# Kernel optimization log

Hardware: AMD Instinct MI355X
Metric: run time of the kernel (lower is better)

The kernel has to match this reference:

```python
import jax, jax.numpy as jnp
import numpy as np

B, T, D, H = 2, 2048, 2048, 32
HD = D // H
# quantization scales (constructor-time attributes in the original repo)
A_PROJ = 3e-4   # q/k/v proj alpha (W8A8B8O8Linear)
A_QK = 2e-5     # qk_bmm alpha (BMM_S8T_S8N_F32T)
A_PV = 1e-2     # pv_bmm alpha (BMM_S8T_S8N_S8T)
A_OUT = 1e-4    # out_proj alpha (W8A8BFP32OFP32Linear)


def _i8(key, shape):
    return jax.random.randint(key, shape, -128, 128, dtype=jnp.int32).astype(jnp.int8)


def setup_inputs() -> dict:
    key = jax.random.key(0)
    ks = jax.random.split(key, 10)
    hidden_states = _i8(ks[0], (B, T, D))
    # causal mask, 0 on/below diagonal, large negative above
    causal = jnp.triu(jnp.full((T, T), -1e9, dtype=jnp.float32), k=1)
    attention_mask = jnp.broadcast_to(causal, (B, 1, T, T))
    return {
        "hidden_states": hidden_states,
        "attention_mask": attention_mask,
        "Wq": _i8(ks[1], (D, D)), "bq": _i8(ks[2], (D,)),
        "Wk": _i8(ks[3], (D, D)), "bk": _i8(ks[4], (D,)),
        "Wv": _i8(ks[5], (D, D)), "bv": _i8(ks[6], (D,)),
        "Wo": _i8(ks[7], (D, D)),
        "bo": jax.random.normal(ks[8], (D,), dtype=jnp.float32),
    }


def _w8a8b8o8(x_i8, W_i8, b_i8, alpha):
    # int8 GEMM -> int32 accum; epilogue: alpha*acc + bias, saturate to int8
    acc = jnp.einsum('btk,nk->btn', x_i8.astype(jnp.int32), W_i8.astype(jnp.int32))
    y = alpha * acc.astype(jnp.float32) + b_i8.astype(jnp.float32)
    return jnp.clip(jnp.round(y), -128, 127).astype(jnp.int8)


def reference(hidden_states, attention_mask, Wq, bq, Wk, bk, Wv, bv, Wo, bo):
    # q/k/v projections: int8 in, int8 out
    q = _w8a8b8o8(hidden_states, Wq, bq, A_PROJ)
    k = _w8a8b8o8(hidden_states, Wk, bk, A_PROJ)
    v = _w8a8b8o8(hidden_states, Wv, bv, A_PROJ)

    def shape(x):  # [B,T,D] -> [B,H,T,HD]
        return x.reshape(B, T, H, HD).transpose(0, 2, 1, 3)

    qh, kh, vh = shape(q), shape(k), shape(v)

    # qk_bmm (BMM_S8T_S8N_F32T): fp32 = alpha * int8 q @ k^T
    attn = A_QK * jnp.einsum('bhtd,bhsd->bhts',
                             qh.astype(jnp.int32), kh.astype(jnp.int32)).astype(jnp.float32)
    attn = attn + attention_mask  # [B,1,T,T] broadcasts over heads
    attn = jnp.maximum(attn, jnp.finfo(jnp.float32).min)
    probs = jax.nn.softmax(attn, axis=-1)

    # quantize probs: p.mul_(127).round_() -> int8
    p_i8 = jnp.clip(jnp.round(probs * 127.0), -128, 127).astype(jnp.int8)

    # pv_bmm (BMM_S8T_S8N_S8T): int8 out = sat(round(alpha * p @ v))
    pv = jnp.einsum('bhts,bhsd->bhtd', p_i8.astype(jnp.int32), vh.astype(jnp.int32))
    attn_out_i8 = jnp.clip(jnp.round(A_PV * pv.astype(jnp.float32)), -128, 127).astype(jnp.int8)

    # [B,H,T,HD] -> [B,T,D]
    attn_out = attn_out_i8.transpose(0, 2, 1, 3).reshape(B, T, D)

    # out_proj (W8A8BFP32OFP32Linear): fp32 = alpha*(x@W^T) + fp32 bias
    acc = jnp.einsum('btk,nk->btn', attn_out.astype(jnp.int32), Wo.astype(jnp.int32))
    out = A_OUT * acc.astype(jnp.float32) + bo
    return out
```

## Files before the change

kernel.cpp:

```cpp
#include <hip/hip_runtime.h>
#include <cstdint>

#define A_PROJ 3e-4f
#define A_QK   2e-5f
#define A_PV   1e-2f
#define A_OUT  1e-4f

#define NB 2
#define NT 2048
#define ND 2048
#define NH 32
#define NHD 64
#define NM (NB*NT)

typedef int v4i __attribute__((ext_vector_type(4)));

__device__ __forceinline__ int8_t sat8(float y) {
  float r = rintf(y);
  r = fminf(fmaxf(r, -128.f), 127.f);
  return (int8_t)(int)r;
}

__device__ __forceinline__ float exp2_fast(float x) {
  return __builtin_amdgcn_exp2f(x);
}

__device__ __forceinline__ void gl2lds16(const int8_t* g, int8_t* l) {
  __builtin_amdgcn_global_load_lds(
      (const __attribute__((address_space(1))) void*)g,
      (__attribute__((address_space(3))) void*)l, 16, 0, 0);
}

__device__ __forceinline__ uint32_t pack_lo4(float f0, float f1, float f2, float f3) {
  uint32_t u0 = __float_as_uint(f0), u1 = __float_as_uint(f1);
  uint32_t u2 = __float_as_uint(f2), u3 = __float_as_uint(f3);
  uint32_t lo = __builtin_amdgcn_perm(u1, u0, 0x04000400u);
  uint32_t hi = __builtin_amdgcn_perm(u3, u2, 0x04000400u);
  return __builtin_amdgcn_perm(hi, lo, 0x05040100u);
}

#define NWW (ND*ND/4)
__global__ void pack_all(const int* __restrict__ X,
                         const int* __restrict__ W0, const int* __restrict__ W1,
                         const int* __restrict__ W2, const int* __restrict__ W3,
                         int8_t* __restrict__ dX, int8_t* __restrict__ dW0,
                         int8_t* __restrict__ dW1, int8_t* __restrict__ dW2,
                         int8_t* __restrict__ dW3) {
  int i = blockIdx.x * blockDim.x + threadIdx.x;
  const int nx = NM*ND/4;
  const int* src; int8_t* dst; int off;
  if (i < nx) { src = X; dst = dX; off = i; }
  else {
    int j = i - nx;
    int r = j >> 20;
    off = j & (NWW - 1);
    src = (r == 0) ? W0 : (r == 1) ? W1 : (r == 2) ? W2 : W3;
    dst = (r == 0) ? dW0 : (r == 1) ? dW1 : (r == 2) ? dW2 : dW3;
  }
  int4 v = ((const int4*)src)[off];
  uint32_t p = (uint32_t)(v.x & 255) | ((uint32_t)(v.y & 255) << 8) |
               ((uint32_t)(v.z & 255) << 16) | ((uint32_t)(v.w & 255) << 24);
  ((uint32_t*)dst)[off] = p;
}

__global__ __launch_bounds__(256) void gemm_qkv(
    const int8_t* __restrict__ X,
    const int8_t* __restrict__ Wq, const int8_t* __restrict__ Wk, const int8_t* __restrict__ Wv,
    const int* __restrict__ bq, const int* __restrict__ bk, const int* __restrict__ bv,
    int8_t* __restrict__ Qh, int8_t* __restrict__ Kh, int8_t* __restrict__ Vt)
{
  __shared__ __align__(16) int8_t As[2][128][64];
  __shared__ __align__(16) int8_t Bs[2][128][64];
  const int z = blockIdx.z;
  const int8_t* W  = (z == 0) ? Wq : ((z == 1) ? Wk : Wv);
  const int* bias  = (z == 0) ? bq : ((z == 1) ? bk : bv);
  const int m0 = blockIdx.x * 128, n0 = blockIdx.y * 128;
  const int tid = threadIdx.x, lane = tid & 63, wave = tid >> 6;
  const int wm = wave >> 1, wn = wave & 1;
  const int l15 = lane & 15, quad = lane >> 4;

  const int srow = lane >> 2;
  const int scol = (((lane & 3) ^ ((lane >> 3) & 3)) * 16);
  const int rqcol = (quad ^ ((l15 >> 1) & 3)) * 16;

  v4i acc[4][4];
  const v4i vzero = {0, 0, 0, 0};
  #pragma unroll
  for (int i = 0; i < 4; ++i)
    #pragma unroll
    for (int j = 0; j < 4; ++j) acc[i][j] = vzero;

  for (int k0 = 0; k0 < ND; k0 += 128) {
    #pragma unroll
    for (int j = 0; j < 8; ++j) {
      int slot = j * 4 + wave;
      int sl = slot & 15;
      int hh = sl >> 3, rblk = sl & 7;
      int row = rblk * 16 + srow;
      if (slot < 16) {
        gl2lds16(&X[(size_t)(m0 + row) * ND + k0 + hh * 64 + scol], &As[hh][rblk * 16][0]);
      } else {
        gl2lds16(&W[(size_t)(n0 + row) * ND + k0 + hh * 64 + scol], &Bs[hh][rblk * 16][0]);
      }
    }
    __syncthreads();
    #pragma unroll
    for (int hh = 0; hh < 2; ++hh) {
      v4i a[4], b[4];
      #pragma unroll
      for (int mt = 0; mt < 4; ++mt) a[mt] = *(const v4i*)&As[hh][wm*64 + mt*16 + l15][rqcol];
      #pragma unroll
      for (int nt = 0; nt < 4; ++nt) b[nt] = *(const v4i*)&Bs[hh][wn*64 + nt*16 + l15][rqcol];
      #pragma unroll
      for (int mt = 0; mt < 4; ++mt)
        #pragma unroll
        for (int nt = 0; nt < 4; ++nt)
          acc[mt][nt] = __builtin_amdgcn_mfma_i32_16x16x64_i8(a[mt], b[nt], acc[mt][nt], 0, 0, 0);
    }
    __syncthreads();
  }

  float bf[4];
  #pragma unroll
  for (int nt = 0; nt < 4; ++nt) bf[nt] = (float)bias[n0 + wn*64 + nt*16 + l15];

  if (z == 2) {
    #pragma unroll
    for (int mt = 0; mt < 4; ++mt)
      #pragma unroll
      for (int nt = 0; nt < 4; ++nt) {
        int tbase = (m0 + wm*64 + mt*16 + quad*4) & (NT - 1);
        int bb = (m0 + wm*64) >> 11;
        int n = n0 + wn*64 + nt*16 + l15;
        int hh = n >> 6, hd = n & (NHD - 1);
        uint32_t pk = 0;
        #pragma unroll
        for (int r = 0; r < 4; ++r) {
          uint32_t q = (uint32_t)(uint8_t)sat8(A_PROJ * (float)acc[mt][nt][r] + bf[nt]);
          pk |= q << (8 * r);
        }
        size_t bh = (size_t)bb * NH + hh;
        *(uint32_t*)&Vt[(bh * NHD + hd) * NT + tbase] = pk;
      }
  } else {
    int8_t* O = (z == 0) ? Qh : Kh;
    #pragma unroll
    for (int mt = 0; mt < 4; ++mt)
      #pragma unroll
      for (int nt = 0; nt < 4; ++nt)
        #pragma unroll
        for (int r = 0; r < 4; ++r) {
          int m = m0 + wm*64 + mt*16 + quad*4 + r;
          int n = n0 + wn*64 + nt*16 + l15;
          int8_t q = sat8(A_PROJ * (float)acc[mt][nt][r] + bf[nt]);
          int bb = m >> 11, t = m & (NT - 1);
          int hh = n >> 6, hd = n & (NHD - 1);
          size_t bh = (size_t)bb * NH + hh;
          O[(bh * NT + t) * NHD + hd] = q;
        }
  }
}

__global__ __launch_bounds__(512, 8) void attn_fused(
    const int8_t* __restrict__ Qh, const int8_t* __restrict__ Kh, const int8_t* __restrict__ Vt,
    int8_t* __restrict__ AO)
{
  __shared__ __align__(16) uint32_t Ps32[8][16][20];
  __shared__ float Lsh[2][4][16];
  __shared__ __align__(16) v4i Comb[1024];

  const int bx = blockIdx.x;
  const int bh = blockIdx.y;
  const int tid = threadIdx.x, lane = tid & 63, wave = tid >> 6;
  const int wlocal = wave & 3, group = wave >> 2;
  const int l15 = lane & 15, quad = lane >> 4;
  const v4i vzero = {0, 0, 0, 0};
  const float MAGIC = 12582912.0f;
  const float C2 = 2.8853900817779268e-05f;

  const int8_t* Qp = Qh + (size_t)bh * NT * NHD;
  const int8_t* Kp = Kh + (size_t)bh * NT * NHD;
  const int8_t* Vp = Vt + (size_t)bh * NHD * NT;
  const int bb = bh >> 5, hhead = bh & (NH - 1);
  const int soff = group * 64;

  for (int half = 0; half < 2; ++half) {
    const int xq = half ? (31 - bx) : bx;
    const int t0 = xq * 64;
    const int sd = xq >> 1;
    const int tme = t0 + wlocal * 16 + l15;
    const bool gmask = (group == (xq & 1));
    const bool gskip = (group == 1) && !(xq & 1);

    v4i qf = *(const v4i*)&Qp[(size_t)(t0 + wlocal * 16 + l15) * NHD + quad * 16];

    float lsum = 0.f;
    for (int st = 0; st <= sd; ++st) {
      if (st == sd && gskip) continue;
      const int s0 = st * 128;
      const int8_t* kb = &Kp[(size_t)(s0 + soff + l15) * NHD + quad * 16];
      if (st == sd && gmask) {
        #pragma unroll
        for (int mt = 0; mt < 4; ++mt) {
          v4i kf = *(const v4i*)(kb + mt * 16 * NHD);
          v4i sa = __builtin_amdgcn_mfma_i32_16x16x64_i8(kf, qf, vzero, 0, 0, 0);
          const int sbase = s0 + soff + mt*16 + quad*4;
          #pragma unroll
          for (int r = 0; r < 4; ++r) {
            float e = exp2_fast(C2 * (float)sa[r]);
            lsum += (sbase + r <= tme) ? e : 0.f;
          }
        }
      } else {
        #pragma unroll
        for (int mt = 0; mt < 4; ++mt) {
          v4i kf = *(const v4i*)(kb + mt * 16 * NHD);
          v4i sa = __builtin_amdgcn_mfma_i32_16x16x64_i8(kf, qf, vzero, 0, 0, 0);
          #pragma unroll
          for (int r = 0; r < 4; ++r) lsum += exp2_fast(C2 * (float)sa[r]);
        }
      }
    }
    lsum += __shfl_xor(lsum, 16, 64);
    lsum += __shfl_xor(lsum, 32, 64);
    if (quad == 0) Lsh[group][wlocal][l15] = lsum;
    __syncthreads();
    lsum += Lsh[group ^ 1][wlocal][l15];
    const float linv = 127.0f / lsum;

    v4i accv[4];
    #pragma unroll
    for (int j = 0; j < 4; ++j) accv[j] = vzero;

    for (int st = 0; st <= sd; ++st) {
      if (st == sd && gskip) continue;
      const int s0 = st * 128;
      const int8_t* kb = &Kp[(size_t)(s0 + soff + l15) * NHD + quad * 16];

      if (st == sd && gmask) {
        #pragma unroll
        for (int mt = 0; mt < 4; ++mt) {
          v4i kf = *(const v4i*)(kb + mt * 16 * NHD);
          v4i sa = __builtin_amdgcn_mfma_i32_16x16x64_i8(kf, qf, vzero, 0, 0, 0);
          const int sbase = s0 + soff + mt*16 + quad*4;
          float f[4];
          #pragma unroll
          for (int r = 0; r < 4; ++r) {
            float e = (sbase + r <= tme) ? exp2_fast(C2 * (float)sa[r]) : 0.f;
            f[r] = fmaf(e, linv, MAGIC);
          }
          Ps32[wave][l15][mt*4 + quad] = pack_lo4(f[0], f[1], f[2], f[3]);
        }
      } else {
        #pragma unroll
        for (int mt = 0; mt < 4; ++mt) {
          v4i kf = *(const v4i*)(kb + mt * 16 * NHD);
          v4i sa = __builtin_amdgcn_mfma_i32_16x16x64_i8(kf, qf, vzero, 0, 0, 0);
          float f[4];
          #pragma unroll
          for (int r = 0; r < 4; ++r) {
            float e = exp2_fast(C2 * (float)sa[r]);
            f[r] = fmaf(e, linv, MAGIC);
          }
          Ps32[wave][l15][mt*4 + quad] = pack_lo4(f[0], f[1], f[2], f[3]);
        }
      }
      v4i ap = *(const v4i*)&Ps32[wave][l15][quad*4];
      const int8_t* vb = &Vp[(size_t)l15 * NT + s0 + (group*4 + quad) * 16];
      #pragma unroll
      for (int nt2 = 0; nt2 < 4; ++nt2) {
        v4i bvv = *(const v4i*)(vb + (size_t)(nt2 * 16) * NT);
        accv[nt2] = __builtin_amdgcn_mfma_i32_16x16x64_i8(ap, bvv, accv[nt2], 0, 0, 0);
      }
    }

    v4i* AccA = &Comb[0];
    v4i* AccB = &Comb[512];
    const int cbase = (wlocal * 64 + lane) * 2;
    if (group == 1) {
      AccA[cbase + 0] = accv[0];  AccA[cbase + 1] = accv[1];
      AccB[cbase + 0] = accv[2];  AccB[cbase + 1] = accv[3];
    }
    __syncthreads();
    if (group == 0) {
      v4i p0 = AccA[cbase + 0], p1 = AccA[cbase + 1];
      v4i p2 = AccB[cbase + 0], p3 = AccB[cbase + 1];
      accv[0] += p0;  accv[1] += p1;  accv[2] += p2;  accv[3] += p3;
      #pragma unroll
      for (int nt2 = 0; nt2 < 4; ++nt2)
        #pragma unroll
        for (int r = 0; r < 4; ++r) {
          int t = t0 + wlocal*16 + quad*4 + r;
          int d = nt2*16 + l15;
          AO[((size_t)bb * NT + t) * ND + hhead * NHD + d] = sat8(A_PV * (float)accv[nt2][r]);
        }
    }
    __syncthreads();
  }
}

__global__ __launch_bounds__(256) void gemm_out(
    const int8_t* __restrict__ X, const int8_t* __restrict__ W,
    const float* __restrict__ bo, float* __restrict__ out)
{
  __shared__ __align__(16) int8_t As[2][128][64];
  __shared__ __align__(16) int8_t Bs[2][128][64];
  const int m0 = blockIdx.x * 128, n0 = blockIdx.y * 128;
  const int tid = threadIdx.x, lane = tid & 63, wave = tid >> 6;
  const int wm = wave >> 1, wn = wave & 1;
  const int l15 = lane & 15, quad = lane >> 4;
  const int srow = lane >> 2;
  const int scol = (((lane & 3) ^ ((lane >> 3) & 3)) * 16);
  const int rqcol = (quad ^ ((l15 >> 1) & 3)) * 16;

  v4i acc[4][4];
  const v4i vzero = {0, 0, 0, 0};
  #pragma unroll
  for (int i = 0; i < 4; ++i)
    #pragma unroll
    for (int j = 0; j < 4; ++j) acc[i][j] = vzero;

  for (int k0 = 0; k0 < ND; k0 += 128) {
    #pragma unroll
    for (int j = 0; j < 8; ++j) {
      int slot = j * 4 + wave;
      int sl = slot & 15;
      int hh = sl >> 3, rblk = sl & 7;
      int row = rblk * 16 + srow;
      if (slot < 16) {
        gl2lds16(&X[(size_t)(m0 + row) * ND + k0 + hh * 64 + scol], &As[hh][rblk * 16][0]);
      } else {
        gl2lds16(&W[(size_t)(n0 + row) * ND + k0 + hh * 64 + scol], &Bs[hh][rblk * 16][0]);
      }
    }
    __syncthreads();
    #pragma unroll
    for (int hh = 0; hh < 2; ++hh) {
      v4i a[4], b[4];
      #pragma unroll
      for (int mt = 0; mt < 4; ++mt) a[mt] = *(const v4i*)&As[hh][wm*64 + mt*16 + l15][rqcol];
      #pragma unroll
      for (int nt = 0; nt < 4; ++nt) b[nt] = *(const v4i*)&Bs[hh][wn*64 + nt*16 + l15][rqcol];
      #pragma unroll
      for (int mt = 0; mt < 4; ++mt)
        #pragma unroll
        for (int nt = 0; nt < 4; ++nt)
          acc[mt][nt] = __builtin_amdgcn_mfma_i32_16x16x64_i8(a[mt], b[nt], acc[mt][nt], 0, 0, 0);
    }
    __syncthreads();
  }

  float bf[4];
  #pragma unroll
  for (int nt = 0; nt < 4; ++nt) bf[nt] = bo[n0 + wn*64 + nt*16 + l15];

  #pragma unroll
  for (int mt = 0; mt < 4; ++mt)
    #pragma unroll
    for (int nt = 0; nt < 4; ++nt)
      #pragma unroll
      for (int r = 0; r < 4; ++r) {
        int m = m0 + wm*64 + mt*16 + quad*4 + r;
        int n = n0 + wn*64 + nt*16 + l15;
        out[(size_t)m * ND + n] = A_OUT * (float)acc[mt][nt][r] + bf[nt];
      }
}

extern "C" void kernel_launch(void* const* d_in, const int* in_sizes, int n_in,
                              void* d_out, int out_size, void* d_ws, size_t ws_size,
                              hipStream_t stream)
{
  const int*   hs  = (const int*)d_in[0];
  const int*   Wq  = (const int*)d_in[2];
  const int*   bq  = (const int*)d_in[3];
  const int*   Wk  = (const int*)d_in[4];
  const int*   bkb = (const int*)d_in[5];
  const int*   Wv  = (const int*)d_in[6];
  const int*   bvb = (const int*)d_in[7];
  const int*   Wo  = (const int*)d_in[8];
  const float* bo  = (const float*)d_in[9];
  float* out = (float*)d_out;

  char* ws = (char*)d_ws;
  const size_t SZ_X = (size_t)NM * ND;
  const size_t SZ_W = (size_t)ND * ND;
  const size_t SZ_H = (size_t)NB * NH * NT * NHD;
  int8_t* Xp  = (int8_t*)ws;
  int8_t* Wqp = (int8_t*)(ws + SZ_X);
  int8_t* Wkp = Wqp + SZ_W;
  int8_t* Wvp = Wkp + SZ_W;
  int8_t* Wop = Wvp + SZ_W;
  int8_t* Qh  = Wop + SZ_W;
  int8_t* Kh  = Qh + SZ_H;
  int8_t* Vt  = Kh + SZ_H;
  int8_t* AO  = Xp;

  const int ntot = (int)(SZ_X/4 + 4 * (SZ_W/4));
  pack_all<<<(ntot + 255) / 256, 256, 0, stream>>>(hs, Wq, Wk, Wv, Wo,
                                                   Xp, Wqp, Wkp, Wvp, Wop);

  gemm_qkv<<<dim3(NM/128, ND/128, 3), 256, 0, stream>>>(Xp, Wqp, Wkp, Wvp, bq, bkb, bvb, Qh, Kh, Vt);
  attn_fused<<<dim3(16, NB*NH), 512, 0, stream>>>(Qh, Kh, Vt, AO);
  gemm_out<<<dim3(NM/128, ND/128), 256, 0, stream>>>(AO, Wop, bo, out);
}
```

Baseline: 374.9 us.

## Restructure causal attention to stage K/V tiles in LDS with double buffering

The attention kernel now gives each block 128 query rows, one 16-row slice per wave, instead of two paired 64-row halves split across two wave groups. K and V tiles are loaded into double-buffered shared memory via gl2lds16 and shared by all waves, replacing per-wave global loads, and the cross-group accumulator combine through shared memory is removed. Block-to-query-tile mapping is permuted by head group to balance causal load. This adds a barrier per step and depends on the grid launch matching 16 query tiles per head, which is not visible here.

```diff
diff --git a/kernel.cpp b/kernel.cpp
--- a/kernel.cpp
+++ b/kernel.cpp
@@ -165,138 +165,148 @@
     const int8_t* __restrict__ Qh, const int8_t* __restrict__ Kh, const int8_t* __restrict__ Vt,
     int8_t* __restrict__ AO)
 {
+  __shared__ __align__(16) int8_t Ksd[2][64][64];
+  __shared__ __align__(16) int8_t Vsd[2][64][64];
   __shared__ __align__(16) uint32_t Ps32[8][16][20];
-  __shared__ float Lsh[2][4][16];
-  __shared__ __align__(16) v4i Comb[1024];
 
   const int bx = blockIdx.x;
   const int bh = blockIdx.y;
   const int tid = threadIdx.x, lane = tid & 63, wave = tid >> 6;
-  const int wlocal = wave & 3, group = wave >> 2;
   const int l15 = lane & 15, quad = lane >> 4;
   const v4i vzero = {0, 0, 0, 0};
   const float MAGIC = 12582912.0f;
   const float C2 = 2.8853900817779268e-05f;
 
+  const int jg = bh >> 4;
+  const int x = (jg == 0) ? bx : (jg == 1) ? (15 - bx)
+              : (jg == 2) ? ((bx + 8) & 15) : ((7 - bx) & 15);
+
   const int8_t* Qp = Qh + (size_t)bh * NT * NHD;
   const int8_t* Kp = Kh + (size_t)bh * NT * NHD;
   const int8_t* Vp = Vt + (size_t)bh * NHD * NT;
   const int bb = bh >> 5, hhead = bh & (NH - 1);
-  const int soff = group * 64;
-
-  for (int half = 0; half < 2; ++half) {
-    const int xq = half ? (31 - bx) : bx;
-    const int t0 = xq * 64;
-    const int sd = xq >> 1;
-    const int tme = t0 + wlocal * 16 + l15;
-    const bool gmask = (group == (xq & 1));
-    const bool gskip = (group == 1) && !(xq & 1);
-
-    v4i qf = *(const v4i*)&Qp[(size_t)(t0 + wlocal * 16 + l15) * NHD + quad * 16];
-
-    float lsum = 0.f;
-    for (int st = 0; st <= sd; ++st) {
-      if (st == sd && gskip) continue;
-      const int s0 = st * 128;
-      const int8_t* kb = &Kp[(size_t)(s0 + soff + l15) * NHD + quad * 16];
-      if (st == sd && gmask) {
+
+  const int t0 = x * 128;
+  const int nsteps = 2 * x + 2;
+  const int tw = t0 + wave * 16;
+  const int tme = tw + l15;
+
+  const int strow = lane >> 2;
+  const int stcol = (((lane & 3) ^ ((lane >> 3) & 3)) * 16);
+  const int fcol  = (quad ^ ((l15 >> 1) & 3)) * 16;
+
+  v4i qf = *(const v4i*)&Qp[(size_t)(tw + l15) * NHD + quad * 16];
+
+  float ls0 = 0.f, ls1 = 0.f, ls2 = 0.f, ls3 = 0.f;
+  if (wave < 4)
+    gl2lds16(&Kp[(size_t)(0 + wave*16 + strow) * NHD + stcol], &Ksd[0][wave*16][0]);
+  __syncthreads();
+  int cur = 0;
+  for (int st = 0; st < nsteps; ++st) {
+    if (st + 1 < nsteps && wave < 4)
+      gl2lds16(&Kp[(size_t)((st+1)*64 + wave*16 + strow) * NHD + stcol],
+               &Ksd[cur ^ 1][wave*16][0]);
+    const int s0 = st * 64;
+    if (s0 <= tw + 15) {
+      v4i kf[4];
+      #pragma unroll
+      for (int mt = 0; mt < 4; ++mt) kf[mt] = *(const v4i*)&Ksd[cur][mt*16 + l15][fcol];
+      if (s0 + 63 <= tw) {
         #pragma unroll
         for (int mt = 0; mt < 4; ++mt) {
-          v4i kf = *(const v4i*)(kb + mt * 16 * NHD);
-          v4i sa = __builtin_amdgcn_mfma_i32_16x16x64_i8(kf, qf, vzero, 0, 0, 0);
-          const int sbase = s0 + soff + mt*16 + quad*4;
-          #pragma unroll
-          for (int r = 0; r < 4; ++r) {
-            float e = exp2_fast(C2 * (float)sa[r]);
-            lsum += (sbase + r <= tme) ? e : 0.f;
-          }
+          v4i sa = __builtin_amdgcn_mfma_i32_16x16x64_i8(kf[mt], qf, vzero, 0, 0, 0);
+          ls0 += exp2_fast(C2 * (float)sa[0]);
+          ls1 += exp2_fast(C2 * (float)sa[1]);
+          ls2 += exp2_fast(C2 * (float)sa[2]);
+          ls3 += exp2_fast(C2 * (float)sa[3]);
         }
       } else {
         #pragma unroll
         for (int mt = 0; mt < 4; ++mt) {
-          v4i kf = *(const v4i*)(kb + mt * 16 * NHD);
-          v4i sa = __builtin_amdgcn_mfma_i32_16x16x64_i8(kf, qf, vzero, 0, 0, 0);
-          #pragma unroll
-          for (int r = 0; r < 4; ++r) lsum += exp2_fast(C2 * (float)sa[r]);
-        }
-      }
-    }
-    lsum += __shfl_xor(lsum, 16, 64);
-    lsum += __shfl_xor(lsum, 32, 64);
-    if (quad == 0) Lsh[group][wlocal][l15] = lsum;
-    __syncthreads();
-    lsum += Lsh[group ^ 1][wlocal][l15];
-    const float linv = 127.0f / lsum;
-
-    v4i accv[4];
-    #pragma unroll
-    for (int j = 0; j < 4; ++j) accv[j] = vzero;
-
-    for (int st = 0; st <= sd; ++st) {
-      if (st == sd && gskip) continue;
-      const int s0 = st * 128;
-      const int8_t* kb = &Kp[(size_t)(s0 + soff + l15) * NHD + quad * 16];
-
-      if (st == sd && gmask) {
+          v4i sa = __builtin_amdgcn_mfma_i32_16x16x64_i8(kf[mt], qf, vzero, 0, 0, 0);
+          const int sb = s0 + mt*16 + quad*4;
+          ls0 += (sb + 0 <= tme) ? exp2_fast(C2 * (float)sa[0]) : 0.f;
+          ls1 += (sb + 1 <= tme) ? exp2_fast(C2 * (float)sa[1]) : 0.f;
+          ls2 += (sb + 2 <= tme) ? exp2_fast(C2 * (float)sa[2]) : 0.f;
+          ls3 += (sb + 3 <= tme) ? exp2_fast(C2 * (float)sa[3]) : 0.f;
+        }
+      }
+    }
+    __syncthreads();
+    cur ^= 1;
+  }
+  float lsum = (ls0 + ls1) + (ls2 + ls3);
+  lsum += __shfl_xor(lsum, 16, 64);
+  lsum += __shfl_xor(lsum, 32, 64);
+  const float linv = 127.0f / lsum;
+
+  v4i accv[4];
+  #pragma unroll
+  for (int jj = 0; jj < 4; ++jj) accv[jj] = vzero;
+
+  if (wave < 4)
+    gl2lds16(&Kp[(size_t)(0 + wave*16 + strow) * NHD + stcol], &Ksd[0][wave*16][0]);
+  else
+    gl2lds16(&Vp[(size_t)((wave-4)*16 + strow) * NT + 0 + stcol], &Vsd[0][(wave-4)*16][0]);
+  __syncthreads();
+  cur = 0;
+  for (int st = 0; st < nsteps; ++st) {
+    if (st + 1 < nsteps) {
+      if (wave < 4)
+        gl2lds16(&Kp[(size_t)((st+1)*64 + wave*16 + strow) * NHD + stcol],
+                 &Ksd[cur ^ 1][wave*16][0]);
+      else
+        gl2lds16(&Vp[(size_t)((wave-4)*16 + strow) * NT + (st+1)*64 + stcol],
+                 &Vsd[cur ^ 1][(wave-4)*16][0]);
+    }
+    const int s0 = st * 64;
+    if (s0 <= tw + 15) {
+      v4i kf[4];
+      #pragma unroll
+      for (int mt = 0; mt < 4; ++mt) kf[mt] = *(const v4i*)&Ksd[cur][mt*16 + l15][fcol];
+      if (s0 + 63 <= tw) {
         #pragma unroll
         for (int mt = 0; mt < 4; ++mt) {
-          v4i kf = *(const v4i*)(kb + mt * 16 * NHD);
-          v4i sa = __builtin_amdgcn_mfma_i32_16x16x64_i8(kf, qf, vzero, 0, 0, 0);
-          const int sbase = s0 + soff + mt*16 + quad*4;
-          float f[4];
-          #pragma unroll
-          for (int r = 0; r < 4; ++r) {
-            float e = (sbase + r <= tme) ? exp2_fast(C2 * (float)sa[r]) : 0.f;
-            f[r] = fmaf(e, linv, MAGIC);
-          }
-          Ps32[wave][l15][mt*4 + quad] = pack_lo4(f[0], f[1], f[2], f[3]);
+          v4i sa = __builtin_amdgcn_mfma_i32_16x16x64_i8(kf[mt], qf, vzero, 0, 0, 0);
+          float f0 = fmaf(exp2_fast(C2 * (float)sa[0]), linv, MAGIC);
+          float f1 = fmaf(exp2_fast(C2 * (float)sa[1]), linv, MAGIC);
+          float f2 = fmaf(exp2_fast(C2 * (float)sa[2]), linv, MAGIC);
+          float f3 = fmaf(exp2_fast(C2 * (float)sa[3]), linv, MAGIC);
+          Ps32[wave][l15][mt*4 + quad] = pack_lo4(f0, f1, f2, f3);
         }
       } else {
         #pragma unroll
         for (int mt = 0; mt < 4; ++mt) {
-          v4i kf = *(const v4i*)(kb + mt * 16 * NHD);
-          v4i sa = __builtin_amdgcn_mfma_i32_16x16x64_i8(kf, qf, vzero, 0, 0, 0);
-          float f[4];
-          #pragma unroll
-          for (int r = 0; r < 4; ++r) {
-            float e = exp2_fast(C2 * (float)sa[r]);
-            f[r] = fmaf(e, linv, MAGIC);
-          }
-          Ps32[wave][l15][mt*4 + quad] = pack_lo4(f[0], f[1], f[2], f[3]);
+          v4i sa = __builtin_amdgcn_mfma_i32_16x16x64_i8(kf[mt], qf, vzero, 0, 0, 0);
+          const int sb = s0 + mt*16 + quad*4;
+          float e0 = (sb + 0 <= tme) ? exp2_fast(C2 * (float)sa[0]) : 0.f;
+          float e1 = (sb + 1 <= tme) ? exp2_fast(C2 * (float)sa[1]) : 0.f;
+          float e2 = (sb + 2 <= tme) ? exp2_fast(C2 * (float)sa[2]) : 0.f;
+          float e3 = (sb + 3 <= tme) ? exp2_fast(C2 * (float)sa[3]) : 0.f;
+          Ps32[wave][l15][mt*4 + quad] =
+              pack_lo4(fmaf(e0, linv, MAGIC), fmaf(e1, linv, MAGIC),
+                       fmaf(e2, linv, MAGIC), fmaf(e3, linv, MAGIC));
         }
       }
       v4i ap = *(const v4i*)&Ps32[wave][l15][quad*4];
-      const int8_t* vb = &Vp[(size_t)l15 * NT + s0 + (group*4 + quad) * 16];
       #pragma unroll
       for (int nt2 = 0; nt2 < 4; ++nt2) {
-        v4i bvv = *(const v4i*)(vb + (size_t)(nt2 * 16) * NT);
+        v4i bvv = *(const v4i*)&Vsd[cur][nt2*16 + l15][fcol];
         accv[nt2] = __builtin_amdgcn_mfma_i32_16x16x64_i8(ap, bvv, accv[nt2], 0, 0, 0);
       }
     }
-
-    v4i* AccA = &Comb[0];
-    v4i* AccB = &Comb[512];
-    const int cbase = (wlocal * 64 + lane) * 2;
-    if (group == 1) {
-      AccA[cbase + 0] = accv[0];  AccA[cbase + 1] = accv[1];
-      AccB[cbase + 0] = accv[2];  AccB[cbase + 1] = accv[3];
-    }
-    __syncthreads();
-    if (group == 0) {
-      v4i p0 = AccA[cbase + 0], p1 = AccA[cbase + 1];
-      v4i p2 = AccB[cbase + 0], p3 = AccB[cbase + 1];
-      accv[0] += p0;  accv[1] += p1;  accv[2] += p2;  accv[3] += p3;
-      #pragma unroll
-      for (int nt2 = 0; nt2 < 4; ++nt2)
-        #pragma unroll
-        for (int r = 0; r < 4; ++r) {
-          int t = t0 + wlocal*16 + quad*4 + r;
-          int d = nt2*16 + l15;
-          AO[((size_t)bb * NT + t) * ND + hhead * NHD + d] = sat8(A_PV * (float)accv[nt2][r]);
-        }
-    }
-    __syncthreads();
-  }
+    __syncthreads();
+    cur ^= 1;
+  }
+
+  #pragma unroll
+  for (int nt2 = 0; nt2 < 4; ++nt2)
+    #pragma unroll
+    for (int r = 0; r < 4; ++r) {
+      int t = tw + quad*4 + r;
+      int d = nt2*16 + l15;
+      AO[((size_t)bb * NT + t) * ND + hhead * NHD + d] = sat8(A_PV * (float)accv[nt2][r]);
+    }
 }
 
 __global__ __launch_bounds__(256) void gemm_out(
```

Result: faster. 314.8 us (-16.0%).
